# Optimization experiments

Hardware: AMD Instinct MI355X
Metric: run time of the kernel (lower is better)

## Reference

```python
import jax, jax.numpy as jnp
import numpy as np

N_NODES = 100000
N_EDGES = 1200000
NODE_IN = 64
EDGE_IN = 32
HIDDEN = 64


def _glorot(key, shape):
    fan_in, fan_out = shape[0], shape[1]
    s = jnp.sqrt(2.0 / (fan_in + fan_out))
    return jax.random.normal(key, shape, dtype=jnp.float32) * s


def setup_inputs() -> dict:
    key = jax.random.key(0)
    ks = jax.random.split(key, 16)
    inp = {
        "x": jax.random.normal(ks[0], (N_NODES, NODE_IN), dtype=jnp.float32),
        "edge_index": jax.random.randint(ks[1], (2, N_EDGES), 0, N_NODES, dtype=jnp.int64),
        "edge_attr": jax.random.normal(ks[2], (N_EDGES, EDGE_IN), dtype=jnp.float32),
        # SAGE layer 0 (in=NODE_IN -> HIDDEN): lin_l (neighbors, has bias), lin_r (root)
        "w_l0": _glorot(ks[3], (NODE_IN, HIDDEN)),
        "w_r0": _glorot(ks[4], (NODE_IN, HIDDEN)),
        "b0": jnp.zeros((HIDDEN,), jnp.float32),
        "ln_g0": jnp.ones((HIDDEN,), jnp.float32),
        "ln_b0": jnp.zeros((HIDDEN,), jnp.float32),
        # SAGE layer 1 (HIDDEN -> HIDDEN)
        "w_l1": _glorot(ks[5], (HIDDEN, HIDDEN)),
        "w_r1": _glorot(ks[6], (HIDDEN, HIDDEN)),
        "b1": jnp.zeros((HIDDEN,), jnp.float32),
        "ln_g1": jnp.ones((HIDDEN,), jnp.float32),
        "ln_b1": jnp.zeros((HIDDEN,), jnp.float32),
        # Edge classifier MLP: in_dim = 3*HIDDEN + EDGE_IN = 224
        "cw1": _glorot(ks[7], (3 * HIDDEN + EDGE_IN, HIDDEN)),
        "cb1": jnp.zeros((HIDDEN,), jnp.float32),
        "cw2": _glorot(ks[8], (HIDDEN, HIDDEN // 2)),
        "cb2": jnp.zeros((HIDDEN // 2,), jnp.float32),
        "cw3": _glorot(ks[9], (HIDDEN // 2, 1)),
        "cb3": jnp.zeros((1,), jnp.float32),
    }
    return inp


def _sage_conv(x, src, dst, w_l, w_r, b):
    # mean-aggregate source features at destination nodes (PyG SAGEConv, aggr='mean')
    n = x.shape[0]
    msg = x[src]  # [E, F] gather
    agg = jax.ops.segment_sum(msg, dst, num_segments=n)
    cnt = jax.ops.segment_sum(jnp.ones((src.shape[0], 1), x.dtype), dst, num_segments=n)
    mean = agg / jnp.maximum(cnt, 1.0)
    return mean @ w_l + x @ w_r + b


def _layer_norm(x, g, b, eps=1e-5):
    mu = jnp.mean(x, axis=-1, keepdims=True)
    var = jnp.var(x, axis=-1, keepdims=True)
    return (x - mu) * jax.lax.rsqrt(var + eps) * g + b


def reference(x, edge_index, edge_attr,
              w_l0, w_r0, b0, ln_g0, ln_b0,
              w_l1, w_r1, b1, ln_g1, ln_b1,
              cw1, cb1, cw2, cb2, cw3, cb3):
    src, dst = edge_index[0], edge_index[1]
    # Encoder (eval mode: dropout is identity)
    h = jax.nn.relu(_layer_norm(_sage_conv(x, src, dst, w_l0, w_r0, b0), ln_g0, ln_b0))
    z = jax.nn.relu(_layer_norm(_sage_conv(h, src, dst, w_l1, w_r1, b1), ln_g1, ln_b1))
    # Edge classifier: gather-concat-MLP
    z_src = z[src]
    z_dst = z[dst]
    edge_repr = jnp.concatenate([z_src, z_dst, z_src * z_dst, edge_attr], axis=-1)
    h1 = jax.nn.relu(edge_repr @ cw1 + cb1)
    h2 = jax.nn.relu(h1 @ cw2 + cb2)
    logits = (h2 @ cw3 + cb3).squeeze(-1)  # [E]
    return logits
```

## Files before the change

kernel.cpp:

```cpp
#include <hip/hip_runtime.h>
#include <hip/hip_bf16.h>

#define N_NODES 100000
#define N_EDGES 1200000

typedef __attribute__((ext_vector_type(8))) short bfrag;
typedef __attribute__((ext_vector_type(4))) float ffrag;

union FragU { uint4 v; uint32_t u[4]; bfrag f; };

__device__ __forceinline__ ushort bfbits(float a) {
  union { __hip_bfloat16 h; ushort u; } c; c.h = __float2bfloat16(a); return c.u;
}
__device__ __forceinline__ uint32_t pkbf(float a, float b) {
  union { __hip_bfloat162 h; uint32_t u; } c;
  c.h = __float22bfloat162_rn(float2{a, b}); return c.u;
}
__device__ __forceinline__ uint32_t mul2bf(uint32_t a, uint32_t b) {
  union { uint32_t u; __hip_bfloat162 h; } x, y, r;
  x.u = a; y.u = b; r.h = __hmul2(x.h, y.h); return r.u;
}
__device__ __forceinline__ float bflo(uint32_t u) { return __int_as_float(u << 16); }
__device__ __forceinline__ float bfhi(uint32_t u) { return __int_as_float(u & 0xffff0000u); }


__global__ void cvt_k(const float* __restrict__ x, ushort* __restrict__ xb, int n2) {
  int i = blockIdx.x * blockDim.x + threadIdx.x;
  if (i < n2) {
    float2 v = ((const float2*)x)[i];
    ((uint32_t*)xb)[i] = pkbf(v.x, v.y);
  }
}


__global__ void hist_k(const int* __restrict__ ei, int* __restrict__ deg,
                       int* __restrict__ rank, int E) {
  int e = blockIdx.x * blockDim.x + threadIdx.x;
  if (e < E) rank[e] = atomicAdd(&deg[ei[E + e]], 1);
}

__global__ __launch_bounds__(1024) void scan1_k(const int* __restrict__ deg,
                                                int* __restrict__ off,
                                                int* __restrict__ bsum, int n) {
  __shared__ int wpart[16];
  __shared__ int wpre[16];
  int tid = threadIdx.x, lane = tid & 63, wid = tid >> 6;
  int i = blockIdx.x * 1024 + tid;
  int v = (i < n) ? deg[i] : 0;
  int x = v;
  #pragma unroll
  for (int o = 1; o < 64; o <<= 1) {
    int y = __shfl_up(x, o);
    if (lane >= o) x += y;
  }
  if (lane == 63) wpart[wid] = x;
  __syncthreads();
  if (tid == 0) {
    int run = 0;
    #pragma unroll
    for (int w = 0; w < 16; w++) { int t = wpart[w]; wpre[w] = run; run += t; }
    bsum[blockIdx.x] = run;
  }
  __syncthreads();
  if (i < n) off[i] = x - v + wpre[wid];
}

__global__ void scan2_k(const int* __restrict__ bsum, int* __restrict__ bpre,
                        int* __restrict__ off, int nb, int n) {
  if (threadIdx.x == 0) {
    int run = 0;
    for (int b = 0; b < nb; b++) { int t = bsum[b]; bpre[b] = run; run += t; }
    off[n] = run;
  }
}

__global__ __launch_bounds__(1024) void scan3_k(int* __restrict__ off,
                                                const int* __restrict__ bpre, int n) {
  int i = blockIdx.x * 1024 + threadIdx.x;
  if (i < n) off[i] += bpre[blockIdx.x];
}

__global__ void fill_k(const int* __restrict__ ei, const int* __restrict__ off,
                       const int* __restrict__ rank, int* __restrict__ csr, int E) {
  int e = blockIdx.x * blockDim.x + threadIdx.x;
  if (e < E) {
    int d = ei[E + e];
    int p = off[d] + rank[e];
    __builtin_nontemporal_store(ei[e], &csr[p]);
  }
}


__global__ __launch_bounds__(256) void agg_k(
    const ushort* __restrict__ Xb, const int* __restrict__ off, const int* __restrict__ csr,
    ushort* __restrict__ aggout, int n) {
  int lane = threadIdx.x & 63;
  int quad = lane >> 4, f8 = lane & 15;
  int wave = blockIdx.x * 4 + (threadIdx.x >> 6);
  int nw = gridDim.x * 4;
  int nquads = (n + 3) >> 2;
  const uint2* X2 = (const uint2*)Xb;
  for (int p = wave; p < nquads; p += nw) {
    int i = p * 4 + quad;
    int ic = i < n ? i : n - 1;
    int s0 = off[ic], s1 = off[ic + 1];
    float a0 = 0.f, a1 = 0.f, a2 = 0.f, a3 = 0.f;
    for (int j = s0; j < s1; j += 8) {
      int id[8]; uint2 us[8];
      #pragma unroll
      for (int u = 0; u < 8; u++) {
        int jj = j + u;
        id[u] = csr[jj < s1 ? jj : s1 - 1];
      }
      #pragma unroll
      for (int u = 0; u < 8; u++) us[u] = X2[(size_t)id[u] * 16 + f8];
      #pragma unroll
      for (int u = 0; u < 8; u++) {
        if (j + u < s1) {
          a0 += bflo(us[u].x); a1 += bfhi(us[u].x);
          a2 += bflo(us[u].y); a3 += bfhi(us[u].y);
        }
      }
    }
    if (i < n) {
      float rdeg = 1.f / fmaxf((float)(s1 - s0), 1.f);
      uint2 w;
      w.x = pkbf(a0 * rdeg, a1 * rdeg);
      w.y = pkbf(a2 * rdeg, a3 * rdeg);
      ((uint2*)aggout)[(size_t)i * 16 + f8] = w;
    }
  }
}


__global__ __launch_bounds__(256) void node_k(
    const ushort* __restrict__ agg, const ushort* __restrict__ selfb,
    const float* __restrict__ wl, const float* __restrict__ wr,
    const float* __restrict__ bias, const float* __restrict__ g, const float* __restrict__ lb,
    ushort* __restrict__ outb, int n) {
  __shared__ ushort wt[64 * 128];
  const int tid = threadIdx.x;
  for (int i = tid; i < 8192; i += 256) {
    int k = i >> 6, nn = i & 63;
    float v = (k < 64) ? wl[k * 64 + nn] : wr[(k - 64) * 64 + nn];
    wt[nn * 128 + (((k >> 3) ^ (nn & 7)) * 8) + (k & 7)] = bfbits(v);
  }
  __syncthreads();
  const int lane = tid & 63, wid = tid >> 6;
  const int ln = lane & 15, q = lane >> 4;
  float bias_n[4], g_n[4], lb_n[4];
  #pragma unroll
  for (int nt = 0; nt < 4; nt++) {
    bias_n[nt] = bias[nt * 16 + ln];
    g_n[nt] = g[nt * 16 + ln];
    lb_n[nt] = lb[nt * 16 + ln];
  }
  const int ntiles = (n + 15) >> 4;
  for (int t = blockIdx.x * 4 + wid; t < ntiles; t += gridDim.x * 4) {
    int node = t * 16 + ln;
    int nc = node < n ? node : n - 1;
    FragU afr[4];
    #pragma unroll
    for (int kk = 0; kk < 2; kk++) {
      afr[kk].v     = ((const uint4*)agg)[(size_t)nc * 8 + kk * 4 + q];
      afr[2 + kk].v = ((const uint4*)selfb)[(size_t)nc * 8 + kk * 4 + q];
    }
    ffrag acc[4];
    #pragma unroll
    for (int nt = 0; nt < 4; nt++) acc[nt] = ffrag{0.f, 0.f, 0.f, 0.f};
    #pragma unroll
    for (int kk = 0; kk < 4; kk++) {
      bfrag a = afr[kk].f;
      #pragma unroll
      for (int nt = 0; nt < 4; nt++) {
        int nn = nt * 16 + ln;
        int b = kk * 4 + q;
        const bfrag* bp = (const bfrag*)&wt[nn * 128 + ((b ^ (nn & 7)) * 8)];
        acc[nt] = __builtin_amdgcn_mfma_f32_16x16x32_bf16(a, *bp, acc[nt], 0, 0, 0);
      }
    }
    #pragma unroll
    for (int r = 0; r < 4; r++) {
      int m = t * 16 + q * 4 + r;
      float o[4];
      #pragma unroll
      for (int nt = 0; nt < 4; nt++) o[nt] = acc[nt][r] + bias_n[nt];
      float s = (o[0] + o[1]) + (o[2] + o[3]);
      #pragma unroll
      for (int mm = 1; mm < 16; mm <<= 1) s += __shfl_xor(s, mm);
      float mu = s * (1.f / 64.f);
      float v2 = 0.f;
      #pragma unroll
      for (int nt = 0; nt < 4; nt++) { float d2 = o[nt] - mu; v2 += d2 * d2; }
      #pragma unroll
      for (int mm = 1; mm < 16; mm <<= 1) v2 += __shfl_xor(v2, mm);
      float rs = rsqrtf(v2 * (1.f / 64.f) + 1e-5f);
      if (m < n) {
        #pragma unroll
        for (int nt = 0; nt < 4; nt++) {
          float y = fmaxf((o[nt] - mu) * rs * g_n[nt] + lb_n[nt], 0.f);
          outb[(size_t)m * 64 + nt * 16 + ln] = bfbits(y);
        }
      }
    }
  }
}


__global__ __launch_bounds__(256) void edge_mfma_k(
    const int* __restrict__ ei, const float* __restrict__ ea,
    const ushort* __restrict__ zb,
    const float* __restrict__ cw1, const float* __restrict__ cb1,
    const float* __restrict__ cw2, const float* __restrict__ cb2,
    const float* __restrict__ cw3, const float* __restrict__ cb3,
    float* __restrict__ out, int E) {
  __shared__ ushort wt1[64 * 256];
  __shared__ ushort h1b[4][16 * 64];
  const int tid = threadIdx.x;

  for (int i = tid; i < 224 * 64; i += 256) {
    int k = i >> 6, n = i & 63;
    int blk = k >> 3;
    wt1[n * 256 + ((blk ^ (n & 7)) * 8) + (k & 7)] = bfbits(cw1[i]);
  }
  __syncthreads();

  const int lane = tid & 63, wid = tid >> 6;
  const int ln = lane & 15, q = lane >> 4;

  float cb1v[4];
  #pragma unroll
  for (int t = 0; t < 4; t++) cb1v[t] = cb1[t * 16 + ln];
  float cb2a = cb2[ln], cb2b = cb2[16 + ln];
  float w3a = cw3[ln], w3b = cw3[16 + ln];
  float cb3v = cb3[0];

  FragU w2f[2][2];
  #pragma unroll
  for (int t2 = 0; t2 < 2; t2++) {
    #pragma unroll
    for (int kk = 0; kk < 2; kk++) {
      #pragma unroll
      for (int p = 0; p < 4; p++) {
        int k = kk * 32 + q * 8 + p * 2;
        int n = t2 * 16 + ln;
        w2f[t2][kk].u[p] = pkbf(cw2[k * 32 + n], cw2[(k + 1) * 32 + n]);
      }
    }
  }

  ushort* hb = h1b[wid];
  const int ntiles = E >> 4;
  const int stride = gridDim.x * 4;
  int t = blockIdx.x * 4 + wid;

  FragU curz[4]; float4 ceal, ceah;
  if (t < ntiles) {
    int e = t * 16 + ln;
    int s = ei[e], d = ei[E + e];
    curz[0].v = ((const uint4*)zb)[(size_t)s * 8 + q];
    curz[1].v = ((const uint4*)zb)[(size_t)s * 8 + 4 + q];
    curz[2].v = ((const uint4*)zb)[(size_t)d * 8 + q];
    curz[3].v = ((const uint4*)zb)[(size_t)d * 8 + 4 + q];
    ceal = ((const float4*)ea)[(size_t)e * 8 + q * 2];
    ceah = ((const float4*)ea)[(size_t)e * 8 + q * 2 + 1];
  }

  for (; t < ntiles; t += stride) {
    int tn = t + stride;
    FragU nz[4]; float4 neal, neah;
    if (tn < ntiles) {
      int e2 = tn * 16 + ln;
      int s2 = ei[e2], d2 = ei[E + e2];
      nz[0].v = ((const uint4*)zb)[(size_t)s2 * 8 + q];
      nz[1].v = ((const uint4*)zb)[(size_t)s2 * 8 + 4 + q];
      nz[2].v = ((const uint4*)zb)[(size_t)d2 * 8 + q];
      nz[3].v = ((const uint4*)zb)[(size_t)d2 * 8 + 4 + q];
      neal = ((const float4*)ea)[(size_t)e2 * 8 + q * 2];
      neah = ((const float4*)ea)[(size_t)e2 * 8 + q * 2 + 1];
    }

    FragU afr[7];
    afr[0] = curz[0]; afr[1] = curz[1]; afr[2] = curz[2]; afr[3] = curz[3];
    #pragma unroll
    for (int kk = 0; kk < 2; kk++) {
      #pragma unroll
      for (int p = 0; p < 4; p++)
        afr[4 + kk].u[p] = mul2bf(curz[kk].u[p], curz[2 + kk].u[p]);
    }
    afr[6].u[0] = pkbf(ceal.x, ceal.y); afr[6].u[1] = pkbf(ceal.z, ceal.w);
    afr[6].u[2] = pkbf(ceah.x, ceah.y); afr[6].u[3] = pkbf(ceah.z, ceah.w);

    ffrag acc1[4];
    #pragma unroll
    for (int tt = 0; tt < 4; tt++) acc1[tt] = ffrag{0.f, 0.f, 0.f, 0.f};
    #pragma unroll
    for (int kk = 0; kk < 7; kk++) {
      bfrag a = afr[kk].f;
      #pragma unroll
      for (int tt = 0; tt < 4; tt++) {
        int n = tt * 16 + ln;
        int b = kk * 4 + q;
        const bfrag* bp = (const bfrag*)&wt1[n * 256 + ((b ^ (n & 7)) * 8)];
        acc1[tt] = __builtin_amdgcn_mfma_f32_16x16x32_bf16(a, *bp, acc1[tt], 0, 0, 0);
      }
    }

    #pragma unroll
    for (int tt = 0; tt < 4; tt++) {
      #pragma unroll
      for (int r = 0; r < 4; r++) {
        int m = q * 4 + r;
        int col = tt * 16 + ln;
        float v = fmaxf(acc1[tt][r] + cb1v[tt], 0.f);
        hb[m * 64 + (((col >> 3) ^ (m & 7)) * 8) + (col & 7)] = bfbits(v);
      }
    }

    ffrag acc2[2];
    acc2[0] = ffrag{0.f, 0.f, 0.f, 0.f};
    acc2[1] = ffrag{0.f, 0.f, 0.f, 0.f};
    #pragma unroll
    for (int kk = 0; kk < 2; kk++) {
      int b = kk * 4 + q;
      const bfrag* ap = (const bfrag*)&hb[ln * 64 + ((b ^ (ln & 7)) * 8)];
      bfrag a2 = *ap;
      acc2[0] = __builtin_amdgcn_mfma_f32_16x16x32_bf16(a2, w2f[0][kk].f, acc2[0], 0, 0, 0);
      acc2[1] = __builtin_amdgcn_mfma_f32_16x16x32_bf16(a2, w2f[1][kk].f, acc2[1], 0, 0, 0);
    }

    float p0, p1, p2, p3;
    {
      p0 = fmaxf(acc2[0][0] + cb2a, 0.f) * w3a + fmaxf(acc2[1][0] + cb2b, 0.f) * w3b;
      p1 = fmaxf(acc2[0][1] + cb2a, 0.f) * w3a + fmaxf(acc2[1][1] + cb2b, 0.f) * w3b;
      p2 = fmaxf(acc2[0][2] + cb2a, 0.f) * w3a + fmaxf(acc2[1][2] + cb2b, 0.f) * w3b;
      p3 = fmaxf(acc2[0][3] + cb2a, 0.f) * w3a + fmaxf(acc2[1][3] + cb2b, 0.f) * w3b;
    }
    #pragma unroll
    for (int o = 1; o < 16; o <<= 1) {
      p0 += __shfl_xor(p0, o);
      p1 += __shfl_xor(p1, o);
      p2 += __shfl_xor(p2, o);
      p3 += __shfl_xor(p3, o);
    }
    float keep = (ln == 0) ? p0 : (ln == 1) ? p1 : (ln == 2) ? p2 : p3;
    if (ln < 4) out[t * 16 + q * 4 + ln] = keep + cb3v;

    curz[0] = nz[0]; curz[1] = nz[1]; curz[2] = nz[2]; curz[3] = nz[3];
    ceal = neal; ceah = neah;
  }
}


extern "C" void kernel_launch(void* const* d_in, const int* in_sizes, int n_in,
                              void* d_out, int out_size, void* d_ws, size_t ws_size,
                              hipStream_t stream) {
  const float* x   = (const float*)d_in[0];
  const int*   ei  = (const int*)d_in[1];
  const float* ea  = (const float*)d_in[2];
  const float* wl0 = (const float*)d_in[3];
  const float* wr0 = (const float*)d_in[4];
  const float* b0  = (const float*)d_in[5];
  const float* g0  = (const float*)d_in[6];
  const float* lb0 = (const float*)d_in[7];
  const float* wl1 = (const float*)d_in[8];
  const float* wr1 = (const float*)d_in[9];
  const float* b1  = (const float*)d_in[10];
  const float* g1  = (const float*)d_in[11];
  const float* lb1 = (const float*)d_in[12];
  const float* cw1 = (const float*)d_in[13];
  const float* cb1 = (const float*)d_in[14];
  const float* cw2 = (const float*)d_in[15];
  const float* cb2 = (const float*)d_in[16];
  const float* cw3 = (const float*)d_in[17];
  const float* cb3 = (const float*)d_in[18];
  float* out = (float*)d_out;
  const int N = N_NODES, E = N_EDGES;
  const int NB = (N + 1023) / 1024;

  uintptr_t pp = (uintptr_t)d_ws;
  auto alloc = [&](size_t bytes) {
    uintptr_t r = (pp + 255) & ~(uintptr_t)255; pp = r + bytes; return (void*)r;
  };
  int* deg  = (int*)alloc((size_t)N * 4);
  int* off  = (int*)alloc((size_t)(N + 1) * 4);
  int* rank = (int*)alloc((size_t)E * 4);
  int* csr  = (int*)alloc((size_t)E * 4);
  int* bsum = (int*)alloc((size_t)NB * 4);
  int* bpre = (int*)alloc((size_t)NB * 4);
  ushort* xb  = (ushort*)alloc((size_t)N * 64 * 2);
  ushort* agg = (ushort*)alloc((size_t)N * 64 * 2);
  ushort* hb  = (ushort*)alloc((size_t)N * 64 * 2);
  ushort* zb  = (ushort*)alloc((size_t)N * 64 * 2);

  hipMemsetAsync(deg, 0, (size_t)N * 4, stream);
  cvt_k<<<(N * 32 + 255) / 256, 256, 0, stream>>>(x, xb, N * 32);
  hist_k<<<(E + 255) / 256, 256, 0, stream>>>(ei, deg, rank, E);
  scan1_k<<<NB, 1024, 0, stream>>>(deg, off, bsum, N);
  scan2_k<<<1, 64, 0, stream>>>(bsum, bpre, off, NB, N);
  scan3_k<<<NB, 1024, 0, stream>>>(off, bpre, N);
  fill_k<<<(E + 255) / 256, 256, 0, stream>>>(ei, off, rank, csr, E);
  agg_k<<<2048, 256, 0, stream>>>(xb, off, csr, agg, N);
  node_k<<<512, 256, 0, stream>>>(agg, xb, wl0, wr0, b0, g0, lb0, hb, N);
  agg_k<<<2048, 256, 0, stream>>>(hb, off, csr, agg, N);
  node_k<<<512, 256, 0, stream>>>(agg, hb, wl1, wr1, b1, g1, lb1, zb, N);
  edge_mfma_k<<<1024, 256, 0, stream>>>(ei, ea, zb, cw1, cb1, cw2, cb2, cw3, cb3, out, E);
}
```

Measured before the change: 511.4 us.

## Stage edge tile gathers through LDS with coalesced loads and index prefetch

The edge classifier now loads each tile's source and destination z rows and edge attributes with a lane layout where eight lanes cover one 128-byte row. It converts edge_attr to bf16 at load time, writes everything into a per-wave swizzled LDS staging buffer, and reads the MFMA fragments back from LDS. Edge indices are prefetched two tiles ahead, the staging buffer is reused for the h1 intermediate, and the grid shrinks from 1024 to 768 blocks. The goal is more coalesced global traffic and deeper latency hiding, paid for with extra LDS writes and reads per tile and a within-wave reuse of the staging buffer that needs care about ordering.

```diff
diff --git a/kernel.cpp b/kernel.cpp
--- a/kernel.cpp
+++ b/kernel.cpp
@@ -207,6 +207,42 @@
 }
 
 
+__device__ __forceinline__ void load_tile_regs(
+    const ushort* __restrict__ zb, const float* __restrict__ ea, int tc,
+    int sv, int dv, int lane, uint4* zr, uint2* er) {
+  int rl = lane >> 3, c = lane & 7;
+  int cs = (c ^ rl) * 8;
+  #pragma unroll
+  for (int i = 0; i < 2; i++) {
+    int su = __shfl(sv, i * 8 + rl);
+    zr[i] = *(const uint4*)&zb[(size_t)su * 64 + cs];
+  }
+  #pragma unroll
+  for (int i = 0; i < 2; i++) {
+    int du = __shfl(dv, i * 8 + rl);
+    zr[2 + i] = *(const uint4*)&zb[(size_t)du * 64 + cs];
+  }
+  #pragma unroll
+  for (int j = 0; j < 2; j++) {
+    float4 f = *(const float4*)&ea[(size_t)tc * 512 + j * 256 + lane * 4];
+    er[j].x = pkbf(f.x, f.y); er[j].y = pkbf(f.z, f.w);
+  }
+}
+
+__device__ __forceinline__ void write_tile_lds(ushort* sb, int lane,
+                                               const uint4* zr, const uint2* er) {
+  int rl = lane >> 3, g = lane & 7;
+  #pragma unroll
+  for (int i = 0; i < 2; i++)
+    *(uint4*)&sb[i * 512 + lane * 8] = zr[i];
+  #pragma unroll
+  for (int i = 0; i < 2; i++)
+    *(uint4*)&sb[1024 + i * 512 + lane * 8] = zr[2 + i];
+  #pragma unroll
+  for (int j = 0; j < 2; j++)
+    *(uint2*)&sb[2048 + (j * 8 + rl) * 32 + ((g ^ (rl & 6)) * 4)] = er[j];
+}
+
 __global__ __launch_bounds__(256) void edge_mfma_k(
     const int* __restrict__ ei, const float* __restrict__ ea,
     const ushort* __restrict__ zb,
@@ -215,7 +251,7 @@
     const float* __restrict__ cw3, const float* __restrict__ cb3,
     float* __restrict__ out, int E) {
   __shared__ ushort wt1[64 * 256];
-  __shared__ ushort h1b[4][16 * 64];
+  __shared__ __align__(16) ushort stg[4][2560];
   const int tid = threadIdx.x;
 
   for (int i = tid; i < 224 * 64; i += 256) {
@@ -227,6 +263,8 @@
 
   const int lane = tid & 63, wid = tid >> 6;
   const int ln = lane & 15, q = lane >> 4;
+  const int lnf = lane & 15;
+  ushort* sb = stg[wid];
 
   float cb1v[4];
   #pragma unroll
@@ -249,54 +287,48 @@
     }
   }
 
-  ushort* hb = h1b[wid];
-  const int ntiles = E >> 4;
-  const int stride = gridDim.x * 4;
+  const int nt = E >> 4;
+  const int S = gridDim.x * 4;
   int t = blockIdx.x * 4 + wid;
-
-  FragU curz[4]; float4 ceal, ceah;
-  if (t < ntiles) {
-    int e = t * 16 + ln;
-    int s = ei[e], d = ei[E + e];
-    curz[0].v = ((const uint4*)zb)[(size_t)s * 8 + q];
-    curz[1].v = ((const uint4*)zb)[(size_t)s * 8 + 4 + q];
-    curz[2].v = ((const uint4*)zb)[(size_t)d * 8 + q];
-    curz[3].v = ((const uint4*)zb)[(size_t)d * 8 + 4 + q];
-    ceal = ((const float4*)ea)[(size_t)e * 8 + q * 2];
-    ceah = ((const float4*)ea)[(size_t)e * 8 + q * 2 + 1];
-  }
-
-  for (; t < ntiles; t += stride) {
-    int tn = t + stride;
-    FragU nz[4]; float4 neal, neah;
-    if (tn < ntiles) {
-      int e2 = tn * 16 + ln;
-      int s2 = ei[e2], d2 = ei[E + e2];
-      nz[0].v = ((const uint4*)zb)[(size_t)s2 * 8 + q];
-      nz[1].v = ((const uint4*)zb)[(size_t)s2 * 8 + 4 + q];
-      nz[2].v = ((const uint4*)zb)[(size_t)d2 * 8 + q];
-      nz[3].v = ((const uint4*)zb)[(size_t)d2 * 8 + 4 + q];
-      neal = ((const float4*)ea)[(size_t)e2 * 8 + q * 2];
-      neah = ((const float4*)ea)[(size_t)e2 * 8 + q * 2 + 1];
-    }
-
-    FragU afr[7];
-    afr[0] = curz[0]; afr[1] = curz[1]; afr[2] = curz[2]; afr[3] = curz[3];
-    #pragma unroll
-    for (int kk = 0; kk < 2; kk++) {
-      #pragma unroll
-      for (int p = 0; p < 4; p++)
-        afr[4 + kk].u[p] = mul2bf(curz[kk].u[p], curz[2 + kk].u[p]);
-    }
-    afr[6].u[0] = pkbf(ceal.x, ceal.y); afr[6].u[1] = pkbf(ceal.z, ceal.w);
-    afr[6].u[2] = pkbf(ceah.x, ceah.y); afr[6].u[3] = pkbf(ceah.z, ceah.w);
+  if (t >= nt) return;
+
+  uint4 zr[4]; uint2 er[2];
+  {
+    int sv0 = ei[t * 16 + lnf], dv0 = ei[E + t * 16 + lnf];
+    load_tile_regs(zb, ea, t, sv0, dv0, lane, zr, er);
+    write_tile_lds(sb, lane, zr, er);
+  }
+  int t1 = t + S < nt ? t + S : nt - 1;
+  int sv = ei[t1 * 16 + lnf], dv = ei[E + t1 * 16 + lnf];
+
+  for (; t < nt; t += S) {
+    int tn = t + S;
+    int tc = tn < nt ? tn : nt - 1;
+    load_tile_regs(zb, ea, tc, sv, dv, lane, zr, er);
+    int t2i = t + 2 * S < nt ? t + 2 * S : nt - 1;
+    int sv2 = ei[t2i * 16 + lnf], dv2 = ei[E + t2i * 16 + lnf];
+
+    const int sw = ln & 7;
+    FragU za[4];
+    za[0].v = *(const uint4*)&sb[(size_t)ln * 64 + ((q ^ sw) * 8)];
+    za[1].v = *(const uint4*)&sb[(size_t)ln * 64 + (((4 + q) ^ sw) * 8)];
+    za[2].v = *(const uint4*)&sb[1024 + (size_t)ln * 64 + ((q ^ sw) * 8)];
+    za[3].v = *(const uint4*)&sb[1024 + (size_t)ln * 64 + (((4 + q) ^ sw) * 8)];
+    FragU eafr;
+    eafr.v = *(const uint4*)&sb[2048 + (size_t)ln * 32 + (((2 * q) ^ (ln & 6)) * 4)];
 
     ffrag acc1[4];
     #pragma unroll
     for (int tt = 0; tt < 4; tt++) acc1[tt] = ffrag{0.f, 0.f, 0.f, 0.f};
     #pragma unroll
     for (int kk = 0; kk < 7; kk++) {
-      bfrag a = afr[kk].f;
+      FragU af;
+      if (kk < 4) af = za[kk];
+      else if (kk < 6) {
+        #pragma unroll
+        for (int p = 0; p < 4; p++) af.u[p] = mul2bf(za[kk - 4].u[p], za[kk - 2].u[p]);
+      } else af = eafr;
+      bfrag a = af.f;
       #pragma unroll
       for (int tt = 0; tt < 4; tt++) {
         int n = tt * 16 + ln;
@@ -306,6 +338,7 @@
       }
     }
 
+    ushort* hb = sb;
     #pragma unroll
     for (int tt = 0; tt < 4; tt++) {
       #pragma unroll
@@ -346,8 +379,8 @@
     float keep = (ln == 0) ? p0 : (ln == 1) ? p1 : (ln == 2) ? p2 : p3;
     if (ln < 4) out[t * 16 + q * 4 + ln] = keep + cb3v;
 
-    curz[0] = nz[0]; curz[1] = nz[1]; curz[2] = nz[2]; curz[3] = nz[3];
-    ceal = neal; ceah = neah;
+    write_tile_lds(sb, lane, zr, er);
+    sv = sv2; dv = dv2;
   }
 }
 
@@ -404,5 +437,5 @@
   node_k<<<512, 256, 0, stream>>>(agg, xb, wl0, wr0, b0, g0, lb0, hb, N);
   agg_k<<<2048, 256, 0, stream>>>(hb, off, csr, agg, N);
   node_k<<<512, 256, 0, stream>>>(agg, hb, wl1, wr1, b1, g1, lb1, zb, N);
-  edge_mfma_k<<<1024, 256, 0, stream>>>(ei, ea, zb, cw1, cb1, cw2, cb2, cw3, cb3, out, E);
-}
+  edge_mfma_k<<<768, 256, 0, stream>>>(ei, ea, zb, cw1, cb1, cw2, cb2, cw3, cb3, out, E);
+}
```

After: 507.9 us. Within noise of the previous version (-0.7%).

## Hold edge MLP layer-1 weights in registers and reuse shared memory for activations

Applied to the files above, without the earlier changes.

The edge classifier kernel now loads all layer-1 weight fragments (7x4 bf16 fragments) from shared memory into registers once, then reuses the same shared buffer as per-wave scratch for the hidden activations. This removes repeated LDS reads in the MFMA loop and reduces the LDS footprint. Edge attributes are packed to bf16 at prefetch time, the lane reductions use DPP instead of shuffles, and the grid is halved with launch bounds of 2 blocks per CU. The large register footprint (112 VGPRs for weights) may cut occupancy and hurt latency hiding for the gathers.

```diff
diff --git a/kernel.cpp b/kernel.cpp
--- a/kernel.cpp
+++ b/kernel.cpp
@@ -22,6 +22,19 @@
 }
 __device__ __forceinline__ float bflo(uint32_t u) { return __int_as_float(u << 16); }
 __device__ __forceinline__ float bfhi(uint32_t u) { return __int_as_float(u & 0xffff0000u); }
+
+template <int CTRL>
+__device__ __forceinline__ float dpp_add16(float v) {
+  int x = __builtin_amdgcn_update_dpp(0, __float_as_int(v), CTRL, 0xF, 0xF, true);
+  return v + __int_as_float(x);
+}
+__device__ __forceinline__ float reduce16(float v) {
+  v = dpp_add16<0xB1>(v);
+  v = dpp_add16<0x4E>(v);
+  v = dpp_add16<0x141>(v);
+  v = dpp_add16<0x140>(v);
+  return v;
+}
 
 
 __global__ void cvt_k(const float* __restrict__ x, ushort* __restrict__ xb, int n2) {
@@ -207,26 +220,38 @@
 }
 
 
-__global__ __launch_bounds__(256) void edge_mfma_k(
+__global__ __launch_bounds__(256, 2) void edge_mfma_k(
     const int* __restrict__ ei, const float* __restrict__ ea,
     const ushort* __restrict__ zb,
     const float* __restrict__ cw1, const float* __restrict__ cb1,
     const float* __restrict__ cw2, const float* __restrict__ cb2,
     const float* __restrict__ cw3, const float* __restrict__ cb3,
     float* __restrict__ out, int E) {
-  __shared__ ushort wt1[64 * 256];
-  __shared__ ushort h1b[4][16 * 64];
+  __shared__ ushort smem[64 * 256];
   const int tid = threadIdx.x;
 
   for (int i = tid; i < 224 * 64; i += 256) {
     int k = i >> 6, n = i & 63;
     int blk = k >> 3;
-    wt1[n * 256 + ((blk ^ (n & 7)) * 8) + (k & 7)] = bfbits(cw1[i]);
+    smem[n * 256 + ((blk ^ (n & 7)) * 8) + (k & 7)] = bfbits(cw1[i]);
   }
   __syncthreads();
 
   const int lane = tid & 63, wid = tid >> 6;
   const int ln = lane & 15, q = lane >> 4;
+
+  FragU w1f[7][4];
+  #pragma unroll
+  for (int kk = 0; kk < 7; kk++) {
+    #pragma unroll
+    for (int tt = 0; tt < 4; tt++) {
+      int n = tt * 16 + ln;
+      int b = kk * 4 + q;
+      w1f[kk][tt].v = *(const uint4*)&smem[n * 256 + ((b ^ (n & 7)) * 8)];
+    }
+  }
+  __syncthreads();
+  ushort* hb = &smem[wid * 1024];
 
   float cb1v[4];
   #pragma unroll
@@ -249,61 +274,60 @@
     }
   }
 
-  ushort* hb = h1b[wid];
-  const int ntiles = E >> 4;
-  const int stride = gridDim.x * 4;
+  const int nt = E >> 4;
+  const int S = gridDim.x * 4;
   int t = blockIdx.x * 4 + wid;
-
-  FragU curz[4]; float4 ceal, ceah;
-  if (t < ntiles) {
+  if (t >= nt) return;
+
+  FragU curz[4]; uint32_t cea[4];
+  {
     int e = t * 16 + ln;
     int s = ei[e], d = ei[E + e];
     curz[0].v = ((const uint4*)zb)[(size_t)s * 8 + q];
     curz[1].v = ((const uint4*)zb)[(size_t)s * 8 + 4 + q];
     curz[2].v = ((const uint4*)zb)[(size_t)d * 8 + q];
     curz[3].v = ((const uint4*)zb)[(size_t)d * 8 + 4 + q];
-    ceal = ((const float4*)ea)[(size_t)e * 8 + q * 2];
-    ceah = ((const float4*)ea)[(size_t)e * 8 + q * 2 + 1];
-  }
-
-  for (; t < ntiles; t += stride) {
-    int tn = t + stride;
-    FragU nz[4]; float4 neal, neah;
-    if (tn < ntiles) {
-      int e2 = tn * 16 + ln;
-      int s2 = ei[e2], d2 = ei[E + e2];
-      nz[0].v = ((const uint4*)zb)[(size_t)s2 * 8 + q];
-      nz[1].v = ((const uint4*)zb)[(size_t)s2 * 8 + 4 + q];
-      nz[2].v = ((const uint4*)zb)[(size_t)d2 * 8 + q];
-      nz[3].v = ((const uint4*)zb)[(size_t)d2 * 8 + 4 + q];
-      neal = ((const float4*)ea)[(size_t)e2 * 8 + q * 2];
-      neah = ((const float4*)ea)[(size_t)e2 * 8 + q * 2 + 1];
-    }
-
-    FragU afr[7];
-    afr[0] = curz[0]; afr[1] = curz[1]; afr[2] = curz[2]; afr[3] = curz[3];
-    #pragma unroll
-    for (int kk = 0; kk < 2; kk++) {
-      #pragma unroll
-      for (int p = 0; p < 4; p++)
-        afr[4 + kk].u[p] = mul2bf(curz[kk].u[p], curz[2 + kk].u[p]);
-    }
-    afr[6].u[0] = pkbf(ceal.x, ceal.y); afr[6].u[1] = pkbf(ceal.z, ceal.w);
-    afr[6].u[2] = pkbf(ceah.x, ceah.y); afr[6].u[3] = pkbf(ceah.z, ceah.w);
+    float4 l0 = ((const float4*)ea)[(size_t)e * 8 + q * 2];
+    float4 l1 = ((const float4*)ea)[(size_t)e * 8 + q * 2 + 1];
+    cea[0] = pkbf(l0.x, l0.y); cea[1] = pkbf(l0.z, l0.w);
+    cea[2] = pkbf(l1.x, l1.y); cea[3] = pkbf(l1.z, l1.w);
+  }
+
+  for (; t < nt; t += S) {
+    int tn = t + S;
+    int tc = tn < nt ? tn : t;
+    FragU nz[4]; uint32_t nea[4];
+    {
+      int e = tc * 16 + ln;
+      int s = ei[e], d = ei[E + e];
+      nz[0].v = ((const uint4*)zb)[(size_t)s * 8 + q];
+      nz[1].v = ((const uint4*)zb)[(size_t)s * 8 + 4 + q];
+      nz[2].v = ((const uint4*)zb)[(size_t)d * 8 + q];
+      nz[3].v = ((const uint4*)zb)[(size_t)d * 8 + 4 + q];
+      float4 l0 = ((const float4*)ea)[(size_t)e * 8 + q * 2];
+      float4 l1 = ((const float4*)ea)[(size_t)e * 8 + q * 2 + 1];
+      nea[0] = pkbf(l0.x, l0.y); nea[1] = pkbf(l0.z, l0.w);
+      nea[2] = pkbf(l1.x, l1.y); nea[3] = pkbf(l1.z, l1.w);
+    }
 
     ffrag acc1[4];
     #pragma unroll
     for (int tt = 0; tt < 4; tt++) acc1[tt] = ffrag{0.f, 0.f, 0.f, 0.f};
     #pragma unroll
     for (int kk = 0; kk < 7; kk++) {
-      bfrag a = afr[kk].f;
-      #pragma unroll
-      for (int tt = 0; tt < 4; tt++) {
-        int n = tt * 16 + ln;
-        int b = kk * 4 + q;
-        const bfrag* bp = (const bfrag*)&wt1[n * 256 + ((b ^ (n & 7)) * 8)];
-        acc1[tt] = __builtin_amdgcn_mfma_f32_16x16x32_bf16(a, *bp, acc1[tt], 0, 0, 0);
-      }
+      FragU af;
+      if (kk < 4) af = curz[kk];
+      else if (kk < 6) {
+        #pragma unroll
+        for (int p = 0; p < 4; p++) af.u[p] = mul2bf(curz[kk - 4].u[p], curz[kk - 2].u[p]);
+      } else {
+        #pragma unroll
+        for (int p = 0; p < 4; p++) af.u[p] = cea[p];
+      }
+      bfrag a = af.f;
+      #pragma unroll
+      for (int tt = 0; tt < 4; tt++)
+        acc1[tt] = __builtin_amdgcn_mfma_f32_16x16x32_bf16(a, w1f[kk][tt].f, acc1[tt], 0, 0, 0);
     }
 
     #pragma unroll
@@ -329,25 +353,16 @@
       acc2[1] = __builtin_amdgcn_mfma_f32_16x16x32_bf16(a2, w2f[1][kk].f, acc2[1], 0, 0, 0);
     }
 
-    float p0, p1, p2, p3;
-    {
-      p0 = fmaxf(acc2[0][0] + cb2a, 0.f) * w3a + fmaxf(acc2[1][0] + cb2b, 0.f) * w3b;
-      p1 = fmaxf(acc2[0][1] + cb2a, 0.f) * w3a + fmaxf(acc2[1][1] + cb2b, 0.f) * w3b;
-      p2 = fmaxf(acc2[0][2] + cb2a, 0.f) * w3a + fmaxf(acc2[1][2] + cb2b, 0.f) * w3b;
-      p3 = fmaxf(acc2[0][3] + cb2a, 0.f) * w3a + fmaxf(acc2[1][3] + cb2b, 0.f) * w3b;
-    }
-    #pragma unroll
-    for (int o = 1; o < 16; o <<= 1) {
-      p0 += __shfl_xor(p0, o);
-      p1 += __shfl_xor(p1, o);
-      p2 += __shfl_xor(p2, o);
-      p3 += __shfl_xor(p3, o);
-    }
+    float p0 = fmaxf(acc2[0][0] + cb2a, 0.f) * w3a + fmaxf(acc2[1][0] + cb2b, 0.f) * w3b;
+    float p1 = fmaxf(acc2[0][1] + cb2a, 0.f) * w3a + fmaxf(acc2[1][1] + cb2b, 0.f) * w3b;
+    float p2 = fmaxf(acc2[0][2] + cb2a, 0.f) * w3a + fmaxf(acc2[1][2] + cb2b, 0.f) * w3b;
+    float p3 = fmaxf(acc2[0][3] + cb2a, 0.f) * w3a + fmaxf(acc2[1][3] + cb2b, 0.f) * w3b;
+    p0 = reduce16(p0); p1 = reduce16(p1); p2 = reduce16(p2); p3 = reduce16(p3);
     float keep = (ln == 0) ? p0 : (ln == 1) ? p1 : (ln == 2) ? p2 : p3;
     if (ln < 4) out[t * 16 + q * 4 + ln] = keep + cb3v;
 
     curz[0] = nz[0]; curz[1] = nz[1]; curz[2] = nz[2]; curz[3] = nz[3];
-    ceal = neal; ceah = neah;
+    cea[0] = nea[0]; cea[1] = nea[1]; cea[2] = nea[2]; cea[3] = nea[3];
   }
 }
 
@@ -404,5 +419,5 @@
   node_k<<<512, 256, 0, stream>>>(agg, xb, wl0, wr0, b0, g0, lb0, hb, N);
   agg_k<<<2048, 256, 0, stream>>>(hb, off, csr, agg, N);
   node_k<<<512, 256, 0, stream>>>(agg, hb, wl1, wr1, b1, g1, lb1, zb, N);
-  edge_mfma_k<<<1024, 256, 0, stream>>>(ei, ea, zb, cw1, cb1, cw2, cb2, cw3, cb3, out, E);
-}
+  edge_mfma_k<<<512, 256, 0, stream>>>(ei, ea, zb, cw1, cb1, cw2, cb2, cw3, cb3, out, E);
+}
```

Result: no change. 509.4 us (-0.4%).
